# Kernel optimization log

Hardware: AMD Instinct MI355X
Metric: run time of the kernel (lower is better)

The kernel has to match this reference:

```python
import math
import jax, jax.numpy as jnp
import numpy as np

B, T, S = 4, 4096, 1024
HID, CTX, EMB, H = 1024, 768, 1024, 16
D = EMB // H  # head_dim = 64


def setup_inputs() -> dict:
    key = jax.random.key(0)
    ks = jax.random.split(key, 7)
    sc = lambda n: 1.0 / math.sqrt(n)
    return {
        "tokens": jax.random.normal(ks[0], (B, T, HID), jnp.float32),
        "context": jax.random.normal(ks[1], (B, S, CTX), jnp.float32),
        "Wq": jax.random.normal(ks[2], (HID, EMB), jnp.float32) * sc(HID),
        "Wk": jax.random.normal(ks[3], (CTX, EMB), jnp.float32) * sc(CTX),
        "Wv": jax.random.normal(ks[4], (CTX, EMB), jnp.float32) * sc(CTX),
        "Wo": jax.random.normal(ks[5], (EMB, HID), jnp.float32) * sc(EMB),
        "bo": jnp.zeros((HID,), jnp.float32),
    }


def reference(tokens, context, Wq, Wk, Wv, Wo, bo):
    # projections (bias-free, as in torch Linear(bias=False))
    Q = tokens @ Wq              # [B,T,EMB]
    K = context @ Wk             # [B,S,EMB]
    V = context @ Wv             # [B,S,EMB]
    # split heads: B T (H D) -> B H T D
    Q = Q.reshape(B, T, H, D).transpose(0, 2, 1, 3)
    K = K.reshape(B, S, H, D).transpose(0, 2, 1, 3)
    V = V.reshape(B, S, H, D).transpose(0, 2, 1, 3)
    scores = jnp.einsum('bhtd,bhsd->bhts', Q, K) / math.sqrt(D)
    attn = jax.nn.softmax(scores, axis=-1)
    ctx = jnp.einsum('bhts,bhsd->bhtd', attn, V)
    ctx = ctx.transpose(0, 2, 1, 3).reshape(B, T, EMB)
    return ctx @ Wo + bo
```

## Files before the change

kernel.cpp:

```cpp
#include <hip/hip_runtime.h>
#include <hip/hip_bf16.h>

#define B_ 4
#define T_ 4096
#define S_ 1024
#define HID_ 1024
#define CTX_ 768
#define EMB_ 1024
#define H_ 16
#define D_ 64

#define QSCALE 0.18033688011112042f

typedef __attribute__((ext_vector_type(8))) short short8;
typedef __attribute__((ext_vector_type(4))) float f32x4;
typedef __attribute__((ext_vector_type(4))) unsigned short us4;
typedef unsigned short ushort_t;

__device__ inline ushort_t f2b(float f) {
  union { float f; unsigned u; } x; x.f = f;
  return (ushort_t)((x.u + 0x7fffu + ((x.u >> 16) & 1u)) >> 16);
}
__device__ inline unsigned cvtpk2(float a, float b) {
  __hip_bfloat162 h = __float22bfloat162_rn(float2{a, b});
  union { __hip_bfloat162 h; unsigned u; } c; c.h = h; return c.u;
}
__device__ inline ushort_t f2b_fast(float f) {
  __hip_bfloat16 h = __float2bfloat16(f);
  union { __hip_bfloat16 h; ushort_t u; } c; c.h = h; return c.u;
}

using gu32p = const __attribute__((address_space(1))) unsigned int*;
using lu32p = __attribute__((address_space(3))) unsigned int*;
__device__ inline void gload16(const ushort_t* g, ushort_t* l) {
  __builtin_amdgcn_global_load_lds((gu32p)(const void*)g, (lu32p)(void*)l, 16, 0, 0);
}

__global__ __launch_bounds__(256) void conv_bf16(const float* __restrict__ in,
                                                 ushort_t* __restrict__ out) {
  const size_t i = ((size_t)blockIdx.x * 256 + threadIdx.x) * 8;
  const float4 a = *(const float4*)(in + i);
  const float4 b = *(const float4*)(in + i + 4);
  uint4 u;
  u.x = cvtpk2(a.x, a.y); u.y = cvtpk2(a.z, a.w);
  u.z = cvtpk2(b.x, b.y); u.w = cvtpk2(b.z, b.w);
  *(uint4*)(out + i) = u;
}

__global__ __launch_bounds__(256) void convT(const float* __restrict__ W,
                                             ushort_t* __restrict__ Wt,
                                             int K, int N) {
  __shared__ float Ls[32][33];
  const int tid = threadIdx.x;
  const int n0 = blockIdx.x * 32, k0 = blockIdx.y * 32;
  const int r = tid >> 3, c4 = (tid & 7) * 4;
  const float4 v = *(const float4*)&W[(size_t)(k0 + r) * N + n0 + c4];
  Ls[r][c4] = v.x; Ls[r][c4 + 1] = v.y; Ls[r][c4 + 2] = v.z; Ls[r][c4 + 3] = v.w;
  __syncthreads();
  us4 o;
  o.x = f2b_fast(Ls[c4][r]);     o.y = f2b_fast(Ls[c4 + 1][r]);
  o.z = f2b_fast(Ls[c4 + 2][r]); o.w = f2b_fast(Ls[c4 + 3][r]);
  *(us4*)&Wt[(size_t)(n0 + r) * K + k0 + c4] = o;
}

template<int EPI>
__global__ __launch_bounds__(256) void gemm128(
    const ushort_t* __restrict__ A, const ushort_t* __restrict__ Bt,
    void* __restrict__ Cp, const float* __restrict__ bias,
    int M, int Kd, int N)
{
  __shared__ ushort_t As[128 * 32];
  __shared__ ushort_t Bs[128 * 32];
  const int tid = threadIdx.x;
  const int bn = blockIdx.x, bm = blockIdx.y;
  const int lane = tid & 63, w = tid >> 6;
  const int lr = lane & 15, lg = lane >> 4;
  const int wr = w >> 1, wc = w & 1;

  f32x4 acc[4][4] = {};

  const int srow = tid >> 2, scol = (tid & 3) * 8;
  const ushort_t* ga = A + (size_t)(bm * 128 + srow) * Kd + scol;
  const ushort_t* gb = Bt + (size_t)(bn * 128 + srow) * Kd + scol;
  ushort_t* la = &As[tid * 8];
  ushort_t* lb = &Bs[tid * 8];
  const size_t rstep = (size_t)64 * Kd;

  for (int k0 = 0; k0 < Kd; k0 += 32) {
    gload16(ga + k0, la);
    gload16(ga + k0 + rstep, la + 2048);
    gload16(gb + k0, lb);
    gload16(gb + k0 + rstep, lb + 2048);
    __syncthreads();
    short8 af[4], bf[4];
#pragma unroll
    for (int m = 0; m < 4; ++m)
      af[m] = *(const short8*)&As[(wr * 64 + m * 16 + lr) * 32 + lg * 8];
#pragma unroll
    for (int n = 0; n < 4; ++n)
      bf[n] = *(const short8*)&Bs[(wc * 64 + n * 16 + lr) * 32 + lg * 8];
#pragma unroll
    for (int m = 0; m < 4; ++m)
#pragma unroll
      for (int n = 0; n < 4; ++n)
        acc[m][n] = __builtin_amdgcn_mfma_f32_16x16x32_bf16(af[m], bf[n], acc[m][n], 0, 0, 0);
    __syncthreads();
  }

  const int row0 = bm * 128 + wr * 64 + lg * 4;
  const int col0 = bn * 128 + wc * 64 + lr;

  if constexpr (EPI == 2) {
    ushort_t* C = (ushort_t*)Cp;
#pragma unroll
    for (int m = 0; m < 4; ++m) {
      const int rbase = row0 + m * 16;
      const int bb = rbase >> 10;
      const int s0 = rbase & (S_ - 1);
#pragma unroll
      for (int n = 0; n < 4; ++n) {
        const int col = col0 + n * 16;
        const int hh = col >> 6, dd = col & 63;
        us4 o;
        o.x = f2b(acc[m][n][0]); o.y = f2b(acc[m][n][1]);
        o.z = f2b(acc[m][n][2]); o.w = f2b(acc[m][n][3]);
        *(us4*)&C[(((size_t)bb * H_ + hh) * D_ + dd) * S_ + s0] = o;
      }
    }
  } else {
    ushort_t* C = (ushort_t*)Cp;
#pragma unroll
    for (int m = 0; m < 4; ++m)
#pragma unroll
      for (int n = 0; n < 4; ++n) {
        const int col = col0 + n * 16;
#pragma unroll
        for (int i = 0; i < 4; ++i)
          C[(size_t)(row0 + m * 16 + i) * N + col] = f2b(acc[m][n][i]);
      }
  }
}

template<int EPI>
__global__ __launch_bounds__(512) void gemm256(
    const ushort_t* __restrict__ A, const ushort_t* __restrict__ Bt,
    void* __restrict__ Cp, const float* __restrict__ bias,
    int M, int Kd, int N)
{
  extern __shared__ ushort_t L[];
  const int tid = threadIdx.x;
  const int lane = tid & 63, wid = tid >> 6;
  const int lr = lane & 15, lg = lane >> 4;
  const int wm = wid >> 2, wn = wid & 3;

  const int cpx = (int)gridDim.x >> 3;
  const int lin = (int)blockIdx.x;
  const int swz = (lin & 7) * cpx + (lin >> 3);
  const int nbn = N >> 8;
  const int bm = swz / nbn, bn = swz % nbn;

  const int sr = tid >> 2;
  const int csrc = (tid & 3) ^ ((sr >> 1) & 3);
  const ushort_t* gA = A + (size_t)(bm * 256 + sr) * Kd + csrc * 8;
  const ushort_t* gB = Bt + (size_t)(bn * 256 + sr) * Kd + csrc * 8;
  const size_t half = (size_t)128 * Kd;
  ushort_t* const dA = L + tid * 8;
  ushort_t* const dB = L + 8192 + tid * 8;

  f32x4 acc[8][4] = {};
  const int NT = Kd >> 5;

#define STAGE256(c) do {                                \
    const int slot_ = ((c) & 3) * 16384;                \
    const int k0_ = (c) << 5;                           \
    gload16(gA + k0_, dA + slot_);                      \
    gload16(gA + k0_ + half, dA + slot_ + 4096);        \
    gload16(gB + k0_, dB + slot_);                      \
    gload16(gB + k0_ + half, dB + slot_ + 4096);        \
  } while (0)

  STAGE256(0); STAGE256(1); STAGE256(2);
  asm volatile("s_waitcnt vmcnt(8)" ::: "memory");
  __builtin_amdgcn_s_barrier();
  __builtin_amdgcn_sched_barrier(0);

  for (int t = 0; t < NT; ++t) {
    if (t + 3 < NT) STAGE256(t + 3);
    const ushort_t* As_ = L + (t & 3) * 16384;
    const ushort_t* Bs_ = As_ + 8192;
    short8 af[8], bf[4];
#pragma unroll
    for (int m = 0; m < 8; ++m) {
      const int row = wm * 128 + m * 16 + lr;
      af[m] = *(const short8*)&As_[row * 32 + (lg ^ ((row >> 1) & 3)) * 8];
    }
#pragma unroll
    for (int n = 0; n < 4; ++n) {
      const int row = wn * 64 + n * 16 + lr;
      bf[n] = *(const short8*)&Bs_[row * 32 + (lg ^ ((row >> 1) & 3)) * 8];
    }
    __builtin_amdgcn_s_setprio(1);
#pragma unroll
    for (int m = 0; m < 8; ++m)
#pragma unroll
      for (int n = 0; n < 4; ++n)
        acc[m][n] = __builtin_amdgcn_mfma_f32_16x16x32_bf16(af[m], bf[n], acc[m][n], 0, 0, 0);
    __builtin_amdgcn_s_setprio(0);
    asm volatile("s_waitcnt vmcnt(8)" ::: "memory");
    __builtin_amdgcn_s_barrier();
    __builtin_amdgcn_sched_barrier(0);
  }
#undef STAGE256

  const int row0 = bm * 256 + wm * 128 + lg * 4;
  const int col0 = bn * 256 + wn * 64 + lr;

  if constexpr (EPI == 3) {
    float* C = (float*)Cp;
#pragma unroll
    for (int n = 0; n < 4; ++n) {
      const int col = col0 + n * 16;
      const float bv = bias[col];
#pragma unroll
      for (int m = 0; m < 8; ++m)
#pragma unroll
        for (int i = 0; i < 4; ++i)
          C[(size_t)(row0 + m * 16 + i) * N + col] = acc[m][n][i] + bv;
    }
  } else {
    ushort_t* C = (ushort_t*)Cp;
#pragma unroll
    for (int m = 0; m < 8; ++m)
#pragma unroll
      for (int n = 0; n < 4; ++n) {
        const int col = col0 + n * 16;
#pragma unroll
        for (int i = 0; i < 4; ++i)
          C[(size_t)(row0 + m * 16 + i) * N + col] = f2b(acc[m][n][i] * QSCALE);
      }
  }
}

__global__ __launch_bounds__(512) void attn_v5(
    const ushort_t* __restrict__ Q, const ushort_t* __restrict__ K,
    const ushort_t* __restrict__ Vt, ushort_t* __restrict__ C)
{
  __shared__ ushort_t Ks[2][64 * 64];
  __shared__ ushort_t Vs[2][64 * 64];
  __shared__ ushort_t Ps[8][16][72];
  const int tid = threadIdx.x;
  const int lane = tid & 63, w = tid >> 6;
  const int lr = lane & 15, lg = lane >> 4;
  const int t0 = blockIdx.x * 256, h = blockIdx.y, b = blockIdx.z;

  short8 qf[2][2];
#pragma unroll
  for (int qs = 0; qs < 2; ++qs) {
    const size_t qrow = (size_t)b * T_ + t0 + w * 32 + qs * 16 + lr;
    const ushort_t* qp = Q + qrow * EMB_ + h * 64;
    qf[qs][0] = *(const short8*)(qp + lg * 8);
    qf[qs][1] = *(const short8*)(qp + 32 + lg * 8);
  }

  short8 ones;
#pragma unroll
  for (int j = 0; j < 8; ++j) ones[j] = (short)0x3F80;

  f32x4 o[2][4] = {};
  f32x4 lacc[2] = {};

  const int srow = tid >> 3, schunk = tid & 7;
  const int sswz = schunk ^ (srow & 7);
  const ushort_t* kg = K + ((size_t)b * S_ + srow) * EMB_ + h * 64 + sswz * 8;
  const ushort_t* vg = Vt + (((size_t)b * H_ + h) * D_ + srow) * S_ + sswz * 8;

  gload16(kg, &Ks[0][tid * 8]);
  gload16(vg, &Vs[0][tid * 8]);

  int cur = 0;
  for (int st = 0; st < S_ / 64; ++st) {
    __syncthreads();
    if (st + 1 < S_ / 64) {
      gload16(kg + (size_t)(st + 1) * 64 * EMB_, &Ks[cur ^ 1][tid * 8]);
      gload16(vg + (st + 1) * 64, &Vs[cur ^ 1][tid * 8]);
    }

    f32x4 sacc[2][4] = {};
    __builtin_amdgcn_s_setprio(1);
#pragma unroll
    for (int c = 0; c < 4; ++c) {
      const int krow = c * 16 + lr;
      const int sw = krow & 7;
      const short8 ka0 = *(const short8*)&Ks[cur][krow * 64 + ((lg ^ sw) * 8)];
      const short8 ka1 = *(const short8*)&Ks[cur][krow * 64 + (((4 + lg) ^ sw) * 8)];
#pragma unroll
      for (int qs = 0; qs < 2; ++qs) {
        sacc[qs][c] = __builtin_amdgcn_mfma_f32_16x16x32_bf16(ka0, qf[qs][0], sacc[qs][c], 0, 0, 0);
        sacc[qs][c] = __builtin_amdgcn_mfma_f32_16x16x32_bf16(ka1, qf[qs][1], sacc[qs][c], 0, 0, 0);
      }
    }
    __builtin_amdgcn_s_setprio(0);

    short8 pa[2][2];
#pragma unroll
    for (int qs = 0; qs < 2; ++qs) {
#pragma unroll
      for (int c = 0; c < 4; ++c) {
        *(unsigned*)&Ps[w][lr][c * 16 + lg * 4] =
            cvtpk2(exp2f(sacc[qs][c][0]), exp2f(sacc[qs][c][1]));
        *(unsigned*)&Ps[w][lr][c * 16 + lg * 4 + 2] =
            cvtpk2(exp2f(sacc[qs][c][2]), exp2f(sacc[qs][c][3]));
      }
      pa[qs][0] = *(const short8*)&Ps[w][lr][lg * 8];
      pa[qs][1] = *(const short8*)&Ps[w][lr][32 + lg * 8];
    }

    __builtin_amdgcn_s_setprio(1);
#pragma unroll
    for (int sh = 0; sh < 2; ++sh) {
#pragma unroll
      for (int dc = 0; dc < 4; ++dc) {
        const int vrow = dc * 16 + lr;
        const int vsw = vrow & 7;
        const short8 vb = *(const short8*)&Vs[cur][vrow * 64 + (((sh * 4 + lg) ^ vsw) * 8)];
        o[0][dc] = __builtin_amdgcn_mfma_f32_16x16x32_bf16(pa[0][sh], vb, o[0][dc], 0, 0, 0);
        o[1][dc] = __builtin_amdgcn_mfma_f32_16x16x32_bf16(pa[1][sh], vb, o[1][dc], 0, 0, 0);
      }
      lacc[0] = __builtin_amdgcn_mfma_f32_16x16x32_bf16(pa[0][sh], ones, lacc[0], 0, 0, 0);
      lacc[1] = __builtin_amdgcn_mfma_f32_16x16x32_bf16(pa[1][sh], ones, lacc[1], 0, 0, 0);
    }
    __builtin_amdgcn_s_setprio(0);

    cur ^= 1;
  }

#pragma unroll
  for (int qs = 0; qs < 2; ++qs) {
#pragma unroll
    for (int i = 0; i < 4; ++i) {
      const float li = 1.0f / lacc[qs][i];
      const size_t trow = (size_t)b * T_ + t0 + w * 32 + qs * 16 + lg * 4 + i;
#pragma unroll
      for (int dc = 0; dc < 4; ++dc)
        C[trow * EMB_ + h * 64 + dc * 16 + lr] = f2b_fast(o[qs][dc][i] * li);
    }
  }
}

extern "C" void kernel_launch(void* const* d_in, const int* in_sizes, int n_in,
                              void* d_out, int out_size, void* d_ws, size_t ws_size,
                              hipStream_t stream) {
  const float* tokens  = (const float*)d_in[0];
  const float* context = (const float*)d_in[1];
  const float* Wq = (const float*)d_in[2];
  const float* Wk = (const float*)d_in[3];
  const float* Wv = (const float*)d_in[4];
  const float* Wo = (const float*)d_in[5];
  const float* bo = (const float*)d_in[6];
  float* out = (float*)d_out;

  ushort_t* Qb  = (ushort_t*)d_out;
  ushort_t* Tok = Qb + (size_t)B_ * T_ * EMB_;
  ushort_t* Kb   = (ushort_t*)d_ws;
  ushort_t* Vtb  = Kb + (size_t)B_ * S_ * EMB_;
  ushort_t* Cb   = Vtb + (size_t)B_ * S_ * EMB_;
  ushort_t* Wbuf = Cb + (size_t)B_ * T_ * EMB_;

  conv_bf16<<<(B_ * T_ * HID_) / 2048, 256, 0, stream>>>(tokens, Tok);
  convT<<<dim3(EMB_ / 32, HID_ / 32), 256, 0, stream>>>(Wq, Wbuf, HID_, EMB_);
  gemm256<1><<<dim3((B_ * T_ / 256) * (EMB_ / 256)), 512, 131072, stream>>>(
      Tok, Wbuf, Qb, nullptr, B_ * T_, HID_, EMB_);
  conv_bf16<<<(B_ * S_ * CTX_) / 2048, 256, 0, stream>>>(context, Cb);
  convT<<<dim3(EMB_ / 32, CTX_ / 32), 256, 0, stream>>>(Wk, Wbuf, CTX_, EMB_);
  gemm128<0><<<dim3(EMB_ / 128, (B_ * S_) / 128), 256, 0, stream>>>(
      Cb, Wbuf, Kb, nullptr, B_ * S_, CTX_, EMB_);
  convT<<<dim3(EMB_ / 32, CTX_ / 32), 256, 0, stream>>>(Wv, Wbuf, CTX_, EMB_);
  gemm128<2><<<dim3(EMB_ / 128, (B_ * S_) / 128), 256, 0, stream>>>(
      Cb, Wbuf, Vtb, nullptr, B_ * S_, CTX_, EMB_);
  attn_v5<<<dim3(T_ / 256, H_, B_), 512, 0, stream>>>(Qb, Kb, Vtb, Cb);
  convT<<<dim3(HID_ / 32, EMB_ / 32), 256, 0, stream>>>(Wo, Wbuf, EMB_, HID_);
  gemm256<3><<<dim3((B_ * T_ / 256) * (HID_ / 256)), 512, 131072, stream>>>(
      Cb, Wbuf, out, bo, B_ * T_, EMB_, HID_);
}
```

Before: 262.0 us.

## Triple-buffer K/V in attention, double query rows per block, remap grid

The attention kernel now gives each wave 64 query rows instead of 32, so each K/V tile in shared memory is reused across twice as many queries. Tiles are triple-buffered with explicit vmcnt waits so a load runs two tiles ahead, and swizzled LDS offsets are precomputed. The grid is flattened and remapped so that groups of adjacent blocks share the same batch and head, which should improve L2 reuse of K/V. The cost is higher register and LDS use per block and half as many blocks, which risks lower occupancy and a thinner tail wave.

```diff
diff --git a/kernel.cpp b/kernel.cpp
--- a/kernel.cpp
+++ b/kernel.cpp
@@ -241,22 +241,27 @@
   }
 }
 
-__global__ __launch_bounds__(512) void attn_v5(
+__global__ __launch_bounds__(512) void attn_v6(
     const ushort_t* __restrict__ Q, const ushort_t* __restrict__ K,
     const ushort_t* __restrict__ Vt, ushort_t* __restrict__ C)
 {
-  __shared__ ushort_t Ks[2][64 * 64];
-  __shared__ ushort_t Vs[2][64 * 64];
-  __shared__ ushort_t Ps[8][16][72];
+  __shared__ ushort_t Ks[3][4096];
+  __shared__ ushort_t Vs[3][4096];
+  __shared__ ushort_t Ps[8][4][16][72];
   const int tid = threadIdx.x;
   const int lane = tid & 63, w = tid >> 6;
   const int lr = lane & 15, lg = lane >> 4;
-  const int t0 = blockIdx.x * 256, h = blockIdx.y, b = blockIdx.z;
-
-  short8 qf[2][2];
-#pragma unroll
-  for (int qs = 0; qs < 2; ++qs) {
-    const size_t qrow = (size_t)b * T_ + t0 + w * 32 + qs * 16 + lr;
+
+  const int bid = (int)blockIdx.x;
+  const int m8 = (bid >> 3) & 7;
+  const int g = (bid & 7) | ((bid >> 6) << 3);
+  const int h = g & 15, b = g >> 4;
+  const int t0 = m8 * 512;
+
+  short8 qf[4][2];
+#pragma unroll
+  for (int qs = 0; qs < 4; ++qs) {
+    const size_t qrow = (size_t)b * T_ + t0 + w * 64 + qs * 16 + lr;
     const ushort_t* qp = Q + qrow * EMB_ + h * 64;
     qf[qs][0] = *(const short8*)(qp + lg * 8);
     qf[qs][1] = *(const short8*)(qp + 32 + lg * 8);
@@ -266,80 +271,101 @@
 #pragma unroll
   for (int j = 0; j < 8; ++j) ones[j] = (short)0x3F80;
 
-  f32x4 o[2][4] = {};
-  f32x4 lacc[2] = {};
+  f32x4 o[4][4] = {};
+  f32x4 lacc[4] = {};
+
+  int offs[4][2];
+#pragma unroll
+  for (int c = 0; c < 4; ++c)
+#pragma unroll
+    for (int hh = 0; hh < 2; ++hh)
+      offs[c][hh] = (c * 16 + lr) * 64 + (((hh * 4 + lg) ^ (lr & 7)) * 8);
 
   const int srow = tid >> 3, schunk = tid & 7;
   const int sswz = schunk ^ (srow & 7);
   const ushort_t* kg = K + ((size_t)b * S_ + srow) * EMB_ + h * 64 + sswz * 8;
   const ushort_t* vg = Vt + (((size_t)b * H_ + h) * D_ + srow) * S_ + sswz * 8;
-
-  gload16(kg, &Ks[0][tid * 8]);
-  gload16(vg, &Vs[0][tid * 8]);
-
-  int cur = 0;
-  for (int st = 0; st < S_ / 64; ++st) {
-    __syncthreads();
-    if (st + 1 < S_ / 64) {
-      gload16(kg + (size_t)(st + 1) * 64 * EMB_, &Ks[cur ^ 1][tid * 8]);
-      gload16(vg + (st + 1) * 64, &Vs[cur ^ 1][tid * 8]);
-    }
-
-    f32x4 sacc[2][4] = {};
-    __builtin_amdgcn_s_setprio(1);
+  ushort_t* const ksd = &Ks[0][0];
+  ushort_t* const vsd = &Vs[0][0];
+
+  auto tile_body = [&](int slot) {
+    const ushort_t* Kb = &Ks[slot][0];
+    const ushort_t* Vb = &Vs[slot][0];
+    short8 ka[4][2];
 #pragma unroll
     for (int c = 0; c < 4; ++c) {
-      const int krow = c * 16 + lr;
-      const int sw = krow & 7;
-      const short8 ka0 = *(const short8*)&Ks[cur][krow * 64 + ((lg ^ sw) * 8)];
-      const short8 ka1 = *(const short8*)&Ks[cur][krow * 64 + (((4 + lg) ^ sw) * 8)];
-#pragma unroll
-      for (int qs = 0; qs < 2; ++qs) {
-        sacc[qs][c] = __builtin_amdgcn_mfma_f32_16x16x32_bf16(ka0, qf[qs][0], sacc[qs][c], 0, 0, 0);
-        sacc[qs][c] = __builtin_amdgcn_mfma_f32_16x16x32_bf16(ka1, qf[qs][1], sacc[qs][c], 0, 0, 0);
-      }
-    }
-    __builtin_amdgcn_s_setprio(0);
-
-    short8 pa[2][2];
-#pragma unroll
-    for (int qs = 0; qs < 2; ++qs) {
+      ka[c][0] = *(const short8*)&Kb[offs[c][0]];
+      ka[c][1] = *(const short8*)&Kb[offs[c][1]];
+    }
+#pragma unroll
+    for (int qs = 0; qs < 4; ++qs) {
+      f32x4 sacc[4] = {};
+      __builtin_amdgcn_s_setprio(1);
 #pragma unroll
       for (int c = 0; c < 4; ++c) {
-        *(unsigned*)&Ps[w][lr][c * 16 + lg * 4] =
-            cvtpk2(exp2f(sacc[qs][c][0]), exp2f(sacc[qs][c][1]));
-        *(unsigned*)&Ps[w][lr][c * 16 + lg * 4 + 2] =
-            cvtpk2(exp2f(sacc[qs][c][2]), exp2f(sacc[qs][c][3]));
-      }
-      pa[qs][0] = *(const short8*)&Ps[w][lr][lg * 8];
-      pa[qs][1] = *(const short8*)&Ps[w][lr][32 + lg * 8];
-    }
-
-    __builtin_amdgcn_s_setprio(1);
+        sacc[c] = __builtin_amdgcn_mfma_f32_16x16x32_bf16(ka[c][0], qf[qs][0], sacc[c], 0, 0, 0);
+        sacc[c] = __builtin_amdgcn_mfma_f32_16x16x32_bf16(ka[c][1], qf[qs][1], sacc[c], 0, 0, 0);
+      }
+      __builtin_amdgcn_s_setprio(0);
+#pragma unroll
+      for (int c = 0; c < 4; ++c) {
+        uint2 pk;
+        pk.x = cvtpk2(exp2f(sacc[c][0]), exp2f(sacc[c][1]));
+        pk.y = cvtpk2(exp2f(sacc[c][2]), exp2f(sacc[c][3]));
+        *(uint2*)&Ps[w][qs][lr][c * 16 + lg * 4] = pk;
+      }
+    }
 #pragma unroll
     for (int sh = 0; sh < 2; ++sh) {
-#pragma unroll
-      for (int dc = 0; dc < 4; ++dc) {
-        const int vrow = dc * 16 + lr;
-        const int vsw = vrow & 7;
-        const short8 vb = *(const short8*)&Vs[cur][vrow * 64 + (((sh * 4 + lg) ^ vsw) * 8)];
-        o[0][dc] = __builtin_amdgcn_mfma_f32_16x16x32_bf16(pa[0][sh], vb, o[0][dc], 0, 0, 0);
-        o[1][dc] = __builtin_amdgcn_mfma_f32_16x16x32_bf16(pa[1][sh], vb, o[1][dc], 0, 0, 0);
-      }
-      lacc[0] = __builtin_amdgcn_mfma_f32_16x16x32_bf16(pa[0][sh], ones, lacc[0], 0, 0, 0);
-      lacc[1] = __builtin_amdgcn_mfma_f32_16x16x32_bf16(pa[1][sh], ones, lacc[1], 0, 0, 0);
-    }
-    __builtin_amdgcn_s_setprio(0);
-
-    cur ^= 1;
-  }
-
-#pragma unroll
-  for (int qs = 0; qs < 2; ++qs) {
+      short8 vb[4];
+#pragma unroll
+      for (int dc = 0; dc < 4; ++dc)
+        vb[dc] = *(const short8*)&Vb[offs[dc][sh]];
+      __builtin_amdgcn_s_setprio(1);
+#pragma unroll
+      for (int qs = 0; qs < 4; ++qs) {
+        const short8 pa = *(const short8*)&Ps[w][qs][lr][sh * 32 + lg * 8];
+#pragma unroll
+        for (int dc = 0; dc < 4; ++dc)
+          o[qs][dc] = __builtin_amdgcn_mfma_f32_16x16x32_bf16(pa, vb[dc], o[qs][dc], 0, 0, 0);
+        lacc[qs] = __builtin_amdgcn_mfma_f32_16x16x32_bf16(pa, ones, lacc[qs], 0, 0, 0);
+      }
+      __builtin_amdgcn_s_setprio(0);
+    }
+  };
+
+  gload16(kg, ksd + tid * 8);
+  gload16(vg, vsd + tid * 8);
+  gload16(kg + (size_t)64 * EMB_, ksd + 4096 + tid * 8);
+  gload16(vg + 64, vsd + 4096 + tid * 8);
+
+  int slc = 0, sls = 2;
+  for (int t = 0; t < 14; ++t) {
+    asm volatile("s_waitcnt vmcnt(2)" ::: "memory");
+    __builtin_amdgcn_s_barrier();
+    __builtin_amdgcn_sched_barrier(0);
+    gload16(kg + (size_t)(t + 2) * 64 * EMB_, ksd + sls * 4096 + tid * 8);
+    gload16(vg + (t + 2) * 64, vsd + sls * 4096 + tid * 8);
+    tile_body(slc);
+    slc = (slc == 2) ? 0 : slc + 1;
+    sls = (sls == 2) ? 0 : sls + 1;
+  }
+  asm volatile("s_waitcnt vmcnt(2)" ::: "memory");
+  __builtin_amdgcn_s_barrier();
+  __builtin_amdgcn_sched_barrier(0);
+  tile_body(slc);
+  slc = (slc == 2) ? 0 : slc + 1;
+  asm volatile("s_waitcnt vmcnt(0)" ::: "memory");
+  __builtin_amdgcn_s_barrier();
+  __builtin_amdgcn_sched_barrier(0);
+  tile_body(slc);
+
+#pragma unroll
+  for (int qs = 0; qs < 4; ++qs) {
 #pragma unroll
     for (int i = 0; i < 4; ++i) {
       const float li = 1.0f / lacc[qs][i];
-      const size_t trow = (size_t)b * T_ + t0 + w * 32 + qs * 16 + lg * 4 + i;
+      const size_t trow = (size_t)b * T_ + t0 + w * 64 + qs * 16 + lg * 4 + i;
 #pragma unroll
       for (int dc = 0; dc < 4; ++dc)
         C[trow * EMB_ + h * 64 + dc * 16 + lr] = f2b_fast(o[qs][dc][i] * li);
@@ -377,7 +403,7 @@
   convT<<<dim3(EMB_ / 32, CTX_ / 32), 256, 0, stream>>>(Wv, Wbuf, CTX_, EMB_);
   gemm128<2><<<dim3(EMB_ / 128, (B_ * S_) / 128), 256, 0, stream>>>(
       Cb, Wbuf, Vtb, nullptr, B_ * S_, CTX_, EMB_);
-  attn_v5<<<dim3(T_ / 256, H_, B_), 512, 0, stream>>>(Qb, Kb, Vtb, Cb);
+  attn_v6<<<dim3((T_ / 512) * H_ * B_), 512, 0, stream>>>(Qb, Kb, Vtb, Cb);
   convT<<<dim3(HID_ / 32, EMB_ / 32), 256, 0, stream>>>(Wo, Wbuf, EMB_, HID_);
   gemm256<3><<<dim3((B_ * T_ / 256) * (HID_ / 256)), 512, 131072, stream>>>(
       Cb, Wbuf, out, bo, B_ * T_, EMB_, HID_);
```

Measured after the change: 276.2 us. 5.4% more time.

## Merge prep conversions into one launch, fuse K/V projection GEMMs, remap attention grid

Applied to the files above, without the earlier changes.

All input and weight bf16 conversions and transposes (tokens, context, Wq, Wk, Wv) now run in one multi-role kernel, and the K and V projections become a single GEMM over a concatenated [2048 x 768] weight with per-column-half epilogues. The aim is to cut kernel launch count and per-launch tail overhead. The attention grid is flattened and remapped so that eight consecutive blocks share a batch and head group, which should change L2 reuse of K/V tiles. It also swaps the rounding conversion for the library bf16 cast and writes P tiles with one 64-bit store instead of two 32-bit stores.

```diff
diff --git a/kernel.cpp b/kernel.cpp
--- a/kernel.cpp
+++ b/kernel.cpp
@@ -36,9 +36,9 @@
   __builtin_amdgcn_global_load_lds((gu32p)(const void*)g, (lu32p)(void*)l, 16, 0, 0);
 }
 
-__global__ __launch_bounds__(256) void conv_bf16(const float* __restrict__ in,
-                                                 ushort_t* __restrict__ out) {
-  const size_t i = ((size_t)blockIdx.x * 256 + threadIdx.x) * 8;
+__device__ inline void conv_body(const float* __restrict__ in, ushort_t* __restrict__ out,
+                                 int blk, int tid) {
+  const size_t i = ((size_t)blk * 256 + tid) * 8;
   const float4 a = *(const float4*)(in + i);
   const float4 b = *(const float4*)(in + i + 4);
   uint4 u;
@@ -47,14 +47,11 @@
   *(uint4*)(out + i) = u;
 }
 
-__global__ __launch_bounds__(256) void convT(const float* __restrict__ W,
-                                             ushort_t* __restrict__ Wt,
-                                             int K, int N) {
-  __shared__ float Ls[32][33];
-  const int tid = threadIdx.x;
-  const int n0 = blockIdx.x * 32, k0 = blockIdx.y * 32;
+__device__ inline void convT_body(const float* __restrict__ W, ushort_t* __restrict__ Wt,
+                                  int K, int tile, int tid, float (*Ls)[33]) {
+  const int n0 = (tile & 31) * 32, k0 = (tile >> 5) * 32;
   const int r = tid >> 3, c4 = (tid & 7) * 4;
-  const float4 v = *(const float4*)&W[(size_t)(k0 + r) * N + n0 + c4];
+  const float4 v = *(const float4*)&W[(size_t)(k0 + r) * 1024 + n0 + c4];
   Ls[r][c4] = v.x; Ls[r][c4 + 1] = v.y; Ls[r][c4 + 2] = v.z; Ls[r][c4 + 3] = v.w;
   __syncthreads();
   us4 o;
@@ -63,14 +60,40 @@
   *(us4*)&Wt[(size_t)(n0 + r) * K + k0 + c4] = o;
 }
 
-template<int EPI>
-__global__ __launch_bounds__(256) void gemm128(
+__global__ __launch_bounds__(256) void prepA(
+    const float* __restrict__ tokens, const float* __restrict__ context,
+    const float* __restrict__ Wq, const float* __restrict__ Wk,
+    const float* __restrict__ Wv,
+    ushort_t* __restrict__ Tok, ushort_t* __restrict__ CtxB,
+    ushort_t* __restrict__ WqT, ushort_t* __restrict__ WkvT)
+{
+  __shared__ float Ls[32][33];
+  const int tid = threadIdx.x;
+  int blk = (int)blockIdx.x;
+  if (blk < 8192) { conv_body(tokens, Tok, blk, tid); return; }
+  blk -= 8192;
+  if (blk < 1536) { conv_body(context, CtxB, blk, tid); return; }
+  blk -= 1536;
+  if (blk < 1024) { convT_body(Wq, WqT, 1024, blk, tid, Ls); return; }
+  blk -= 1024;
+  if (blk < 768)  { convT_body(Wk, WkvT, 768, blk, tid, Ls); return; }
+  blk -= 768;
+  convT_body(Wv, WkvT + (size_t)1024 * 768, 768, blk, tid, Ls);
+}
+
+__global__ __launch_bounds__(256) void prepO(const float* __restrict__ Wo,
+                                             ushort_t* __restrict__ WoT) {
+  __shared__ float Ls[32][33];
+  convT_body(Wo, WoT, 1024, (int)blockIdx.x, threadIdx.x, Ls);
+}
+
+__global__ __launch_bounds__(256) void gemm128kv(
     const ushort_t* __restrict__ A, const ushort_t* __restrict__ Bt,
-    void* __restrict__ Cp, const float* __restrict__ bias,
-    int M, int Kd, int N)
+    ushort_t* __restrict__ Kb, ushort_t* __restrict__ Vtb)
 {
   __shared__ ushort_t As[128 * 32];
   __shared__ ushort_t Bs[128 * 32];
+  const int Kd = CTX_;
   const int tid = threadIdx.x;
   const int bn = blockIdx.x, bm = blockIdx.y;
   const int lane = tid & 63, w = tid >> 6;
@@ -110,8 +133,17 @@
   const int row0 = bm * 128 + wr * 64 + lg * 4;
   const int col0 = bn * 128 + wc * 64 + lr;
 
-  if constexpr (EPI == 2) {
-    ushort_t* C = (ushort_t*)Cp;
+  if (col0 < 1024) {
+#pragma unroll
+    for (int m = 0; m < 4; ++m)
+#pragma unroll
+      for (int n = 0; n < 4; ++n) {
+        const int col = col0 + n * 16;
+#pragma unroll
+        for (int i = 0; i < 4; ++i)
+          Kb[(size_t)(row0 + m * 16 + i) * EMB_ + col] = f2b_fast(acc[m][n][i]);
+      }
+  } else {
 #pragma unroll
     for (int m = 0; m < 4; ++m) {
       const int rbase = row0 + m * 16;
@@ -119,25 +151,14 @@
       const int s0 = rbase & (S_ - 1);
 #pragma unroll
       for (int n = 0; n < 4; ++n) {
-        const int col = col0 + n * 16;
-        const int hh = col >> 6, dd = col & 63;
+        const int vc = col0 + n * 16 - 1024;
+        const int hh = vc >> 6, dd = vc & 63;
         us4 o;
-        o.x = f2b(acc[m][n][0]); o.y = f2b(acc[m][n][1]);
-        o.z = f2b(acc[m][n][2]); o.w = f2b(acc[m][n][3]);
-        *(us4*)&C[(((size_t)bb * H_ + hh) * D_ + dd) * S_ + s0] = o;
-      }
-    }
-  } else {
-    ushort_t* C = (ushort_t*)Cp;
-#pragma unroll
-    for (int m = 0; m < 4; ++m)
-#pragma unroll
-      for (int n = 0; n < 4; ++n) {
-        const int col = col0 + n * 16;
-#pragma unroll
-        for (int i = 0; i < 4; ++i)
-          C[(size_t)(row0 + m * 16 + i) * N + col] = f2b(acc[m][n][i]);
-      }
+        o.x = f2b_fast(acc[m][n][0]); o.y = f2b_fast(acc[m][n][1]);
+        o.z = f2b_fast(acc[m][n][2]); o.w = f2b_fast(acc[m][n][3]);
+        *(us4*)&Vtb[(((size_t)bb * H_ + hh) * D_ + dd) * S_ + s0] = o;
+      }
+    }
   }
 }
 
@@ -241,7 +262,7 @@
   }
 }
 
-__global__ __launch_bounds__(512) void attn_v5(
+__global__ __launch_bounds__(512) void attn_v5r(
     const ushort_t* __restrict__ Q, const ushort_t* __restrict__ K,
     const ushort_t* __restrict__ Vt, ushort_t* __restrict__ C)
 {
@@ -251,7 +272,12 @@
   const int tid = threadIdx.x;
   const int lane = tid & 63, w = tid >> 6;
   const int lr = lane & 15, lg = lane >> 4;
-  const int t0 = blockIdx.x * 256, h = blockIdx.y, b = blockIdx.z;
+
+  const int bid = (int)blockIdx.x;
+  const int g = (bid & 7) | (((bid >> 3) >> 4) << 3);
+  const int tb = (bid >> 3) & 15;
+  const int h = g & 15, b = g >> 4;
+  const int t0 = tb * 256;
 
   short8 qf[2][2];
 #pragma unroll
@@ -306,10 +332,10 @@
     for (int qs = 0; qs < 2; ++qs) {
 #pragma unroll
       for (int c = 0; c < 4; ++c) {
-        *(unsigned*)&Ps[w][lr][c * 16 + lg * 4] =
-            cvtpk2(exp2f(sacc[qs][c][0]), exp2f(sacc[qs][c][1]));
-        *(unsigned*)&Ps[w][lr][c * 16 + lg * 4 + 2] =
-            cvtpk2(exp2f(sacc[qs][c][2]), exp2f(sacc[qs][c][3]));
+        uint2 pk;
+        pk.x = cvtpk2(exp2f(sacc[qs][c][0]), exp2f(sacc[qs][c][1]));
+        pk.y = cvtpk2(exp2f(sacc[qs][c][2]), exp2f(sacc[qs][c][3]));
+        *(uint2*)&Ps[w][lr][c * 16 + lg * 4] = pk;
       }
       pa[qs][0] = *(const short8*)&Ps[w][lr][lg * 8];
       pa[qs][1] = *(const short8*)&Ps[w][lr][32 + lg * 8];
@@ -364,21 +390,16 @@
   ushort_t* Kb   = (ushort_t*)d_ws;
   ushort_t* Vtb  = Kb + (size_t)B_ * S_ * EMB_;
   ushort_t* Cb   = Vtb + (size_t)B_ * S_ * EMB_;
-  ushort_t* Wbuf = Cb + (size_t)B_ * T_ * EMB_;
-
-  conv_bf16<<<(B_ * T_ * HID_) / 2048, 256, 0, stream>>>(tokens, Tok);
-  convT<<<dim3(EMB_ / 32, HID_ / 32), 256, 0, stream>>>(Wq, Wbuf, HID_, EMB_);
+  ushort_t* WqT  = Cb + (size_t)B_ * T_ * EMB_;
+  ushort_t* WkvT = WqT + (size_t)EMB_ * HID_;
+
+  prepA<<<12288, 256, 0, stream>>>(tokens, context, Wq, Wk, Wv,
+                                   Tok, Cb, WqT, WkvT);
   gemm256<1><<<dim3((B_ * T_ / 256) * (EMB_ / 256)), 512, 131072, stream>>>(
-      Tok, Wbuf, Qb, nullptr, B_ * T_, HID_, EMB_);
-  conv_bf16<<<(B_ * S_ * CTX_) / 2048, 256, 0, stream>>>(context, Cb);
-  convT<<<dim3(EMB_ / 32, CTX_ / 32), 256, 0, stream>>>(Wk, Wbuf, CTX_, EMB_);
-  gemm128<0><<<dim3(EMB_ / 128, (B_ * S_) / 128), 256, 0, stream>>>(
-      Cb, Wbuf, Kb, nullptr, B_ * S_, CTX_, EMB_);
-  convT<<<dim3(EMB_ / 32, CTX_ / 32), 256, 0, stream>>>(Wv, Wbuf, CTX_, EMB_);
-  gemm128<2><<<dim3(EMB_ / 128, (B_ * S_) / 128), 256, 0, stream>>>(
-      Cb, Wbuf, Vtb, nullptr, B_ * S_, CTX_, EMB_);
-  attn_v5<<<dim3(T_ / 256, H_, B_), 512, 0, stream>>>(Qb, Kb, Vtb, Cb);
-  convT<<<dim3(HID_ / 32, EMB_ / 32), 256, 0, stream>>>(Wo, Wbuf, EMB_, HID_);
+      Tok, WqT, Qb, nullptr, B_ * T_, HID_, EMB_);
+  prepO<<<1024, 256, 0, stream>>>(Wo, WqT);
+  gemm128kv<<<dim3(16, 32), 256, 0, stream>>>(Cb, WkvT, Kb, Vtb);
+  attn_v5r<<<dim3((T_ / 256) * H_ * B_), 512, 0, stream>>>(Qb, Kb, Vtb, Cb);
   gemm256<3><<<dim3((B_ * T_ / 256) * (HID_ / 256)), 512, 131072, stream>>>(
-      Cb, Wbuf, out, bo, B_ * T_, EMB_, HID_);
-}
+      Cb, WqT, out, bo, B_ * T_, EMB_, HID_);
+}
```

Measured after the change: 229.5 us. -12.4%, faster.
